# Optimization experiments

Measured on AMD Instinct MI355X. Metric: run time of the kernel, lower is better.

The kernel has to match this reference:

```python
import jax, jax.numpy as jnp
import numpy as np

L = 3          # encoder layers
H, D = 12, 64  # heads, head_dim
DM = H * D     # 768
DF = 3072
WH = WW = 14
S = WH * WW + 1            # 197 tokens incl. cls
ND = (2*WH-1)*(2*WW-1) + 3  # 732 rel-pos entries
EPS = 1e-12


def _make_rel_idx():
    coords = np.stack(np.meshgrid(np.arange(WH), np.arange(WW), indexing='ij'))
    coords = coords.reshape(2, -1)                      # [2, 196]
    rel = (coords[:, :, None] - coords[:, None, :]).transpose(1, 2, 0)  # [196,196,2]
    rel[:, :, 0] += WH - 1
    rel[:, :, 1] += WW - 1
    rel[:, :, 0] *= 2 * WW - 1
    idx = np.zeros((S, S), dtype=np.int32)
    idx[1:, 1:] = rel.sum(-1)
    idx[0, :] = ND - 3
    idx[:, 0] = ND - 2
    idx[0, 0] = ND - 1
    return jnp.asarray(idx.flatten())

REL_IDX = _make_rel_idx()


def _ln(x, g, b):
    m = jnp.mean(x, -1, keepdims=True)
    v = jnp.mean(jnp.square(x - m), -1, keepdims=True)
    return (x - m) * jax.lax.rsqrt(v + EPS) * g + b


def setup_inputs() -> dict:
    key = jax.random.key(0)
    ks = iter(jax.random.split(key, 32))
    p = lambda *s: jax.random.normal(next(ks), s, jnp.float32) * 0.02
    inp = {
        'x': jax.random.normal(next(ks), (64, WH, WW, DM), jnp.float32),
        'cls': p(1, 1, DM),
        'g1': jnp.ones((L, DM)), 'b1': jnp.zeros((L, DM)),
        'Wq': p(L, DM, DM), 'bq': jnp.zeros((L, DM)),
        'Wk': p(L, DM, DM),
        'Wv': p(L, DM, DM), 'bv': jnp.zeros((L, DM)),
        'rel_tbl': p(L, ND, H),
        'Wo': p(L, DM, DM), 'bo': jnp.zeros((L, DM)),
        'lam1': jnp.full((L, DM), 0.1),
        'g2': jnp.ones((L, DM)), 'b2': jnp.zeros((L, DM)),
        'Wi': p(L, DM, DF), 'bi': jnp.zeros((L, DF)),
        'Wmo': p(L, DF, DM), 'bmo': jnp.zeros((L, DM)),
        'lam2': jnp.full((L, DM), 0.1),
    }
    return inp


def reference(x, cls, g1, b1, Wq, bq, Wk, Wv, bv, rel_tbl, Wo, bo, lam1,
              g2, b2, Wi, bi, Wmo, bmo, lam2):
    B = x.shape[0]
    # patchemb: NHWC -> NCHW -> [B, C, HW] -> [B, HW, C], prepend cls token
    t = jnp.transpose(x, (0, 3, 1, 2)).reshape(B, DM, WH * WW)
    t = jnp.transpose(t, (0, 2, 1))
    h = jnp.concatenate([jnp.broadcast_to(cls, (B, 1, DM)), t], axis=1)  # [B,S,DM]

    scale = 1.0 / np.sqrt(D)
    for i in range(L):
        r = h
        hn = _ln(h, g1[i], b1[i])
        q = (hn @ Wq[i] + bq[i]).reshape(B, S, H, D)
        k = (hn @ Wk[i]).reshape(B, S, H, D)
        v = (hn @ Wv[i] + bv[i]).reshape(B, S, H, D)
        scores = jnp.einsum('bqhd,bkhd->bhqk', q, k) * scale   # [B,H,S,S]
        rel = rel_tbl[i][REL_IDX].reshape(S, S, H)             # gather bias table
        scores = scores + jnp.transpose(rel, (2, 0, 1))[None]
        probs = jax.nn.softmax(scores, axis=-1)
        ctx = jnp.einsum('bhqk,bkhd->bqhd', probs, v).reshape(B, S, DM)
        h = r + (ctx @ Wo[i] + bo[i]) * lam1[i]
        r = h
        hn = _ln(h, g2[i], b2[i])
        ff = jax.nn.gelu(hn @ Wi[i] + bi[i], approximate=False) @ Wmo[i] + bmo[i]
        h = r + ff * lam2[i]
    return h  # final encoder output [B, S, DM]
```

## Files before the change

### kernel.cpp

```cpp
#include <hip/hip_runtime.h>

#define DMM 768
#define DFF 3072
#define NH  12
#define HD  64
#define SQ  197
#define BA  64
#define NDD 732
#define MROWS (BA*SQ)
#define MPAD  12672
#define PCOLS 224
#define KS2   72
#define VTS   232
#define QS    2304

typedef unsigned short u16;
typedef __bf16 bf16x8 __attribute__((ext_vector_type(8)));
typedef float  f32x4  __attribute__((ext_vector_type(4)));
typedef unsigned short us8 __attribute__((ext_vector_type(8)));

__device__ __forceinline__ float b2f(u16 u) {
    unsigned v = ((unsigned)u) << 16;
    float f; __builtin_memcpy(&f, &v, 4); return f;
}
__device__ __forceinline__ u16 f2b(float f) {
    unsigned v; __builtin_memcpy(&v, &f, 4);
    unsigned r = v + 0x7FFFu + ((v >> 16) & 1u);
    return (u16)(r >> 16);
}
__device__ __forceinline__ float gelu_exact(float x) {
    return 0.5f * x * (1.0f + erff(x * 0.70710678118654752f));
}
__device__ __forceinline__ void gload16(const u16* g, u16* l) {
    __builtin_amdgcn_global_load_lds(
        (const __attribute__((address_space(1))) unsigned int*)(g),
        (__attribute__((address_space(3))) unsigned int*)(l), 16, 0, 0);
}
__device__ __forceinline__ void hard_barrier() {
    asm volatile("s_waitcnt lgkmcnt(0)" ::: "memory");
    __builtin_amdgcn_s_barrier();
}

__global__ void patch_k(const float* __restrict__ x, const float* __restrict__ cls,
                        float* __restrict__ h) {
    long idx = (long)blockIdx.x * 256 + threadIdx.x;
    if (idx >= (long)MPAD * DMM) return;
    long r = idx / DMM; int c = (int)(idx % DMM);
    float v = 0.0f;
    if (r < MROWS) {
        int b = (int)(r / SQ), s = (int)(r % SQ);
        v = (s == 0) ? cls[c] : x[((long)b * 196 + (s - 1)) * DMM + c];
    }
    h[idx] = v;
}

__global__ void out_k(const float* __restrict__ h, float* __restrict__ out) {
    long idx = (long)blockIdx.x * 256 + threadIdx.x;
    if (idx < (long)MROWS * DMM) out[idx] = h[idx];
}

__global__ __launch_bounds__(256) void tcast_k(const float* __restrict__ in,
                                               u16* __restrict__ out,
                                               int Kd, int Nd) {
    __shared__ float t[32][33];
    int k0 = blockIdx.x * 32, n0 = blockIdx.y * 32;
    int tx = threadIdx.x & 31, ty = threadIdx.x >> 5;
    #pragma unroll
    for (int i = 0; i < 4; ++i)
        t[tx][ty + 8 * i] = in[(long)(k0 + ty + 8 * i) * Nd + n0 + tx];
    __syncthreads();
    #pragma unroll
    for (int i = 0; i < 4; ++i)
        out[(long)(n0 + ty + 8 * i) * Kd + k0 + tx] = f2b(t[ty + 8 * i][tx]);
}

__global__ __launch_bounds__(256) void ln_k(const float* __restrict__ h,
                                            const float* __restrict__ g,
                                            const float* __restrict__ b,
                                            u16* __restrict__ hn) {
    int row = blockIdx.x, tid = threadIdx.x;
    const float* hr = h + (long)row * DMM;
    float x0 = hr[tid], x1 = hr[tid + 256], x2 = hr[tid + 512];
    float s = x0 + x1 + x2, sq = x0 * x0 + x1 * x1 + x2 * x2;
    #pragma unroll
    for (int m = 32; m > 0; m >>= 1) {
        s  += __shfl_xor(s,  m, 64);
        sq += __shfl_xor(sq, m, 64);
    }
    __shared__ float ls[4], lq[4];
    int w = tid >> 6;
    if ((tid & 63) == 0) { ls[w] = s; lq[w] = sq; }
    __syncthreads();
    s  = ls[0] + ls[1] + ls[2] + ls[3];
    sq = lq[0] + lq[1] + lq[2] + lq[3];
    float mean = s * (1.0f / DMM);
    float var  = fmaxf(sq * (1.0f / DMM) - mean * mean, 0.0f);
    float rs = rsqrtf(var + 1e-12f);
    u16* hnr = hn + (long)row * DMM;
    hnr[tid]       = f2b((x0 - mean) * rs * g[tid]       + b[tid]);
    hnr[tid + 256] = f2b((x1 - mean) * rs * g[tid + 256] + b[tid + 256]);
    hnr[tid + 512] = f2b((x2 - mean) * rs * g[tid + 512] + b[tid + 512]);
}

__global__ void bqkv_k(const float* __restrict__ bq, const float* __restrict__ bv,
                       float* __restrict__ out) {
    int i = blockIdx.x * 256 + threadIdx.x;
    if (i >= QS) return;
    out[i] = (i < 768) ? bq[i] : ((i < 1536) ? 0.0f : bv[i - 1536]);
}

template <int EPI>
__global__ __launch_bounds__(256) void gemm_bt(
    const u16* __restrict__ A, const u16* __restrict__ BT,
    const float* __restrict__ bias, u16* __restrict__ outB,
    float* __restrict__ hio, const float* __restrict__ lam,
    int K, int N) {
    __shared__ __align__(16) u16 pool[3 * 8192];
    int tid = threadIdx.x;
    int w = tid >> 6, lane = tid & 63;
    int wr = w >> 1, wc = w & 1;
    int m16 = lane & 15;
    int kq  = (lane >> 4) * 8;
    int kq4 = (lane >> 4) * 4;

    int nwg = gridDim.x, bid = blockIdx.x;
    int qd = nwg >> 3, rm = nwg & 7;
    int xcd = bid & 7, seq = bid >> 3;
    int wg = (xcd < rm ? xcd * (qd + 1) : rm * (qd + 1) + (xcd - rm) * qd) + seq;
    int ntn = N >> 7;
    long m0 = (long)(wg / ntn) * 128;
    long n0 = (long)(wg % ntn) * 128;

    f32x4 acc[4][4] = {};

    int row_a = tid >> 2;
    int col_a = (tid & 3) * 8;
    const u16* gA0 = &A[(m0 + row_a) * (long)K + col_a];
    const u16* gA1 = &A[(m0 + 64 + row_a) * (long)K + col_a];
    const u16* gB0 = &BT[(n0 + row_a) * (long)K + col_a];
    const u16* gB1 = &BT[(n0 + 64 + row_a) * (long)K + col_a];
    int wo = w * 512;

    auto stage = [&](int k, u16* buf) {
        int k0 = k << 5;
        gload16(gA0 + k0, buf + wo);
        gload16(gA1 + k0, buf + 2048 + wo);
        gload16(gB0 + k0, buf + 4096 + wo);
        gload16(gB1 + k0, buf + 6144 + wo);
    };
    auto compute = [&](const u16* buf) {
        bf16x8 af[4], bf[4];
        #pragma unroll
        for (int i = 0; i < 4; ++i)
            af[i] = *(const bf16x8*)&buf[(wr * 64 + i * 16 + m16) * 32 + kq];
        #pragma unroll
        for (int j = 0; j < 4; ++j)
            bf[j] = *(const bf16x8*)&buf[4096 + (wc * 64 + j * 16 + m16) * 32 + kq];
        #pragma unroll
        for (int i = 0; i < 4; ++i)
            #pragma unroll
            for (int j = 0; j < 4; ++j)
                acc[i][j] = __builtin_amdgcn_mfma_f32_16x16x32_bf16(
                    af[i], bf[j], acc[i][j], 0, 0, 0);
    };

    const int nsteps = K >> 5;
    stage(0, pool);
    stage(1, pool + 8192);
    u16* sb = pool + 16384;
    u16* cb = pool;
    for (int ks = 0; ks < nsteps - 2; ++ks) {
        asm volatile("s_waitcnt vmcnt(4) lgkmcnt(0)" ::: "memory");
        __builtin_amdgcn_s_barrier();
        stage(ks + 2, sb);
        compute(cb);
        sb = cb;
        cb = (cb == pool + 16384) ? pool : cb + 8192;
    }
    asm volatile("s_waitcnt vmcnt(4) lgkmcnt(0)" ::: "memory");
    __builtin_amdgcn_s_barrier();
    compute(cb);
    cb = (cb == pool + 16384) ? pool : cb + 8192;
    asm volatile("s_waitcnt vmcnt(0) lgkmcnt(0)" ::: "memory");
    __builtin_amdgcn_s_barrier();
    compute(cb);

    hard_barrier();
    float* Cs = (float*)pool;
    float bcol[4];
    #pragma unroll
    for (int j = 0; j < 4; ++j)
        bcol[j] = bias ? bias[n0 + wc * 64 + j * 16 + m16] : 0.0f;
    int et4 = tid * 4;
    int colr = et4 & 127;
    f32x4 lam4 = {};
    if (EPI == 2) lam4 = *(const f32x4*)&lam[n0 + colr];

    #pragma unroll
    for (int p = 0; p < 2; ++p) {
        if (p) hard_barrier();
        if (wr == p) {
            #pragma unroll
            for (int i = 0; i < 4; ++i)
                #pragma unroll
                for (int j = 0; j < 4; ++j)
                    #pragma unroll
                    for (int r = 0; r < 4; ++r)
                        Cs[(i * 16 + kq4 + r) * 132 + wc * 64 + j * 16 + m16] =
                            acc[i][j][r] + bcol[j];
        }
        hard_barrier();
        #pragma unroll
        for (int k = 0; k < 8; ++k) {
            int e0 = k * 1024 + et4;
            int row = e0 >> 7;
            f32x4 v = *(const f32x4*)&Cs[row * 132 + colr];
            long gi = (m0 + p * 64 + row) * (long)N + n0 + colr;
            if (EPI == 0) {
                uint2 o;
                o.x = (unsigned)f2b(v[0]) | ((unsigned)f2b(v[1]) << 16);
                o.y = (unsigned)f2b(v[2]) | ((unsigned)f2b(v[3]) << 16);
                *(uint2*)&outB[gi] = o;
            } else if (EPI == 1) {
                uint2 o;
                o.x = (unsigned)f2b(gelu_exact(v[0])) | ((unsigned)f2b(gelu_exact(v[1])) << 16);
                o.y = (unsigned)f2b(gelu_exact(v[2])) | ((unsigned)f2b(gelu_exact(v[3])) << 16);
                *(uint2*)&outB[gi] = o;
            } else {
                f32x4 hv = *(f32x4*)&hio[gi];
                #pragma unroll
                for (int t = 0; t < 4; ++t) hv[t] += v[t] * lam4[t];
                *(f32x4*)&hio[gi] = hv;
            }
        }
    }
}

__device__ __forceinline__ int relidx(int q, int k) {
    if (q == 0 && k == 0) return NDD - 1;
    if (k == 0) return NDD - 2;
    if (q == 0) return NDD - 3;
    int a = q - 1, c = k - 1;
    int dh = a / 14 - c / 14 + 13;
    int dw = a % 14 - c % 14 + 13;
    return dh * 27 + dw;
}

__global__ void bias_k(const float* __restrict__ rel, float* __restrict__ bias) {
    int idx = blockIdx.x * 256 + threadIdx.x;
    if (idx >= NH * 208 * 208) return;
    int hh = idx / (208 * 208);
    int r = (idx / 208) % 208, c = idx % 208;
    float v = 0.0f;
    if (r < SQ && c < SQ) v = rel[relidx(r, c) * NH + hh];
    bias[idx] = v;
}

__global__ __launch_bounds__(256) void attn_qk(
    const u16* __restrict__ QKV, const float* __restrict__ bias,
    u16* __restrict__ P) {
    int bh = blockIdx.x;
    int b = bh / NH, hh = bh % NH;
    __shared__ u16 Ks[208 * KS2];
    int tid = threadIdx.x, w = tid >> 6, lane = tid & 63;
    long base = ((long)b * SQ) * QS + hh * HD;
    const u16* Qp = QKV;
    const u16* Kp = QKV + 768;
    u16* Pb = P + (long)bh * 208 * PCOLS;
    for (int idx = tid; idx < 208 * 16; idx += 256)
        Pb[(idx >> 4) * PCOLS + 208 + (idx & 15)] = 0;
    for (int idx = tid; idx < 208 * 8; idx += 256) {
        int row = idx >> 3, dg = (idx & 7) * 8;
        us8 kv = {};
        if (row < SQ) kv = *(const us8*)&Kp[base + (long)row * QS + dg];
        *(us8*)&Ks[row * KS2 + dg] = kv;
    }
    __syncthreads();
    int m16 = lane & 15, quad = lane >> 4;
    int kq8 = quad * 8, q4 = quad * 4;
    const float* bh_bias = bias + (long)hh * 208 * 208;
    for (int t = w; t < 13; t += 4) {
        int m0 = t * 16;
        int qrow = m0 + m16; if (qrow > SQ - 1) qrow = SQ - 1;
        bf16x8 a0 = *(const bf16x8*)&Qp[base + (long)qrow * QS + kq8];
        bf16x8 a1 = *(const bf16x8*)&Qp[base + (long)qrow * QS + 32 + kq8];
        f32x4 sc[13];
        #pragma unroll
        for (int n = 0; n < 13; ++n) {
            bf16x8 b0 = *(const bf16x8*)&Ks[(n * 16 + m16) * KS2 + kq8];
            bf16x8 b1 = *(const bf16x8*)&Ks[(n * 16 + m16) * KS2 + 32 + kq8];
            f32x4 z = {};
            z = __builtin_amdgcn_mfma_f32_16x16x32_bf16(a0, b0, z, 0, 0, 0);
            z = __builtin_amdgcn_mfma_f32_16x16x32_bf16(a1, b1, z, 0, 0, 0);
            sc[n] = z;
        }
        float mx[4] = {-3e38f, -3e38f, -3e38f, -3e38f};
        #pragma unroll
        for (int n = 0; n < 13; ++n) {
            int col = n * 16 + m16;
            bool valid = col < SQ;
            #pragma unroll
            for (int r = 0; r < 4; ++r) {
                float v = sc[n][r] * 0.125f + bh_bias[(m0 + q4 + r) * 208 + col];
                v = valid ? v : -3e38f;
                sc[n][r] = v;
                mx[r] = fmaxf(mx[r], v);
            }
        }
        #pragma unroll
        for (int r = 0; r < 4; ++r)
            #pragma unroll
            for (int msk = 1; msk < 16; msk <<= 1)
                mx[r] = fmaxf(mx[r], __shfl_xor(mx[r], msk, 64));
        float sum[4] = {0, 0, 0, 0};
        #pragma unroll
        for (int n = 0; n < 13; ++n)
            #pragma unroll
            for (int r = 0; r < 4; ++r) {
                float e = __expf(sc[n][r] - mx[r]);
                sc[n][r] = e;
                sum[r] += e;
            }
        #pragma unroll
        for (int r = 0; r < 4; ++r)
            #pragma unroll
            for (int msk = 1; msk < 16; msk <<= 1)
                sum[r] += __shfl_xor(sum[r], msk, 64);
        float inv[4];
        #pragma unroll
        for (int r = 0; r < 4; ++r) inv[r] = 1.0f / sum[r];
        #pragma unroll
        for (int n = 0; n < 13; ++n) {
            int col = n * 16 + m16;
            #pragma unroll
            for (int r = 0; r < 4; ++r)
                Pb[(m0 + q4 + r) * PCOLS + col] = f2b(sc[n][r] * inv[r]);
        }
    }
}

__global__ __launch_bounds__(256) void attn_pv(
    const u16* __restrict__ P, const u16* __restrict__ QKV,
    u16* __restrict__ ctx) {
    int bh = blockIdx.x;
    int b = bh / NH, hh = bh % NH;
    __shared__ u16 Vt[64 * VTS];
    int tid = threadIdx.x, w = tid >> 6, lane = tid & 63;
    long base  = ((long)b * SQ) * QS + 1536 + hh * HD;
    long basec = ((long)b * SQ) * DMM + hh * HD;
    const u16* Vp = QKV;
    for (int idx = tid; idx < 224 * 8; idx += 256) {
        int row = idx >> 3, dg = (idx & 7) * 8;
        us8 vv = {};
        if (row < SQ) vv = *(const us8*)&Vp[base + (long)row * QS + dg];
        #pragma unroll
        for (int j = 0; j < 8; ++j) Vt[(dg + j) * VTS + row] = vv[j];
    }
    __syncthreads();
    const u16* Pb = P + (long)bh * 208 * PCOLS;
    int m16 = lane & 15, quad = lane >> 4;
    int kq8 = quad * 8, q4 = quad * 4;
    for (int t = w; t < 13; t += 4) {
        int m0 = t * 16;
        f32x4 co[4] = {};
        #pragma unroll
        for (int ks = 0; ks < 7; ++ks) {
            bf16x8 ap = *(const bf16x8*)&Pb[(m0 + m16) * PCOLS + ks * 32 + kq8];
            #pragma unroll
            for (int n = 0; n < 4; ++n) {
                bf16x8 bv = *(const bf16x8*)&Vt[(n * 16 + m16) * VTS + ks * 32 + kq8];
                co[n] = __builtin_amdgcn_mfma_f32_16x16x32_bf16(ap, bv, co[n], 0, 0, 0);
            }
        }
        #pragma unroll
        for (int n = 0; n < 4; ++n) {
            int col = n * 16 + m16;
            #pragma unroll
            for (int r = 0; r < 4; ++r) {
                int qr = m0 + q4 + r;
                if (qr < SQ) ctx[basec + (long)qr * DMM + col] = f2b(co[n][r]);
            }
        }
    }
}

extern "C" void kernel_launch(void* const* d_in, const int* in_sizes, int n_in,
                              void* d_out, int out_size, void* d_ws, size_t ws_size,
                              hipStream_t stream) {
    const float* x    = (const float*)d_in[0];
    const float* cls  = (const float*)d_in[1];
    const float* g1   = (const float*)d_in[2];
    const float* b1   = (const float*)d_in[3];
    const float* Wq   = (const float*)d_in[4];
    const float* bq   = (const float*)d_in[5];
    const float* Wk   = (const float*)d_in[6];
    const float* Wv   = (const float*)d_in[7];
    const float* bv   = (const float*)d_in[8];
    const float* rel  = (const float*)d_in[9];
    const float* Wo   = (const float*)d_in[10];
    const float* bo   = (const float*)d_in[11];
    const float* lam1 = (const float*)d_in[12];
    const float* g2   = (const float*)d_in[13];
    const float* b2   = (const float*)d_in[14];
    const float* Wi   = (const float*)d_in[15];
    const float* bi   = (const float*)d_in[16];
    const float* Wmo  = (const float*)d_in[17];
    const float* bmo  = (const float*)d_in[18];
    const float* lam2 = (const float*)d_in[19];

    char* p = (char*)d_ws;
    auto alloc = [&](size_t bytes) -> void* {
        void* r = (void*)p;
        p += (bytes + 255) & ~(size_t)255;
        return r;
    };
    float* h     = (float*)alloc((size_t)MPAD * DMM * 4);
    u16*   hn    = (u16*)alloc((size_t)MPAD * DMM * 2);
    u16*   qkvb  = (u16*)alloc((size_t)MPAD * QS * 2);
    u16*   ffh   = (u16*)alloc((size_t)MPAD * DFF * 2);
    u16*   WqkvT = (u16*)alloc((size_t)QS * DMM * 2);
    u16*   WoT   = (u16*)alloc((size_t)DMM * DMM * 2);
    u16*   WiT   = (u16*)alloc((size_t)DMM * DFF * 2);
    u16*   WmoT  = (u16*)alloc((size_t)DFF * DMM * 2);
    float* biasb = (float*)alloc((size_t)NH * 208 * 208 * 4);
    float* bqkv  = (float*)alloc((size_t)QS * 4);
    u16*   ctxb  = hn;
    u16*   Pbuf  = ffh;

    patch_k<<<((long)MPAD * DMM + 255) / 256, 256, 0, stream>>>(x, cls, h);

    dim3 tg1(DMM / 32, DMM / 32);
    dim3 tg2(DMM / 32, DFF / 32);
    dim3 tg3(DFF / 32, DMM / 32);
    int gqkv = (MPAD / 128) * (QS / 128);
    int g6   = (MPAD / 128) * (DMM / 128);
    int g24  = (MPAD / 128) * (DFF / 128);

    for (int i = 0; i < 3; ++i) {
        size_t wofs  = (size_t)i * DMM * DMM;
        size_t wofs2 = (size_t)i * DMM * DFF;
        tcast_k<<<tg1, 256, 0, stream>>>(Wq + wofs, WqkvT,                 DMM, DMM);
        tcast_k<<<tg1, 256, 0, stream>>>(Wk + wofs, WqkvT + 768 * DMM,     DMM, DMM);
        tcast_k<<<tg1, 256, 0, stream>>>(Wv + wofs, WqkvT + 2 * 768 * DMM, DMM, DMM);
        tcast_k<<<tg1, 256, 0, stream>>>(Wo + wofs, WoT, DMM, DMM);
        tcast_k<<<tg2, 256, 0, stream>>>(Wi + wofs2, WiT, DMM, DFF);
        tcast_k<<<tg3, 256, 0, stream>>>(Wmo + wofs2, WmoT, DFF, DMM);
        bias_k<<<(NH * 208 * 208 + 255) / 256, 256, 0, stream>>>(rel + (size_t)i * NDD * NH, biasb);
        bqkv_k<<<(QS + 255) / 256, 256, 0, stream>>>(bq + i * DMM, bv + i * DMM, bqkv);

        ln_k<<<MPAD, 256, 0, stream>>>(h, g1 + i * DMM, b1 + i * DMM, hn);
        gemm_bt<0><<<gqkv, 256, 0, stream>>>(hn, WqkvT, bqkv, qkvb, nullptr, nullptr, DMM, QS);
        attn_qk<<<BA * NH, 256, 0, stream>>>(qkvb, biasb, Pbuf);
        attn_pv<<<BA * NH, 256, 0, stream>>>(Pbuf, qkvb, ctxb);
        gemm_bt<2><<<g6, 256, 0, stream>>>(ctxb, WoT, bo + i * DMM, nullptr, h, lam1 + i * DMM, DMM, DMM);
        ln_k<<<MPAD, 256, 0, stream>>>(h, g2 + i * DMM, b2 + i * DMM, hn);
        gemm_bt<1><<<g24, 256, 0, stream>>>(hn, WiT, bi + i * DFF, ffh, nullptr, nullptr, DMM, DFF);
        gemm_bt<2><<<g6, 256, 0, stream>>>(ffh, WmoT, bmo + i * DMM, nullptr, h, lam2 + i * DMM, DFF, DMM);
    }

    out_k<<<((long)MROWS * DMM + 255) / 256, 256, 0, stream>>>(h, (float*)d_out);
}
```

Measured before the change: 1.471 ms.

## Switch GEMM from triple-buffered to double-buffered LDS pipeline

Replaces the three-slot rotating LDS buffer in the bf16 GEMM with two fixed buffers and an unrolled-by-two main loop. Each compute is now followed by a full barrier before its buffer is refilled. This shrinks the LDS footprint to about 33 KB, which may let more workgroups share a CU. The cost is a shallower prefetch (one tile ahead instead of two) and extra barriers per K step, so global load latency is less hidden.

Result: faster. 1.383 ms (-6.0%).

```diff
diff --git a/kernel.cpp b/kernel.cpp
--- a/kernel.cpp
+++ b/kernel.cpp
@@ -115,7 +115,7 @@
     const float* __restrict__ bias, u16* __restrict__ outB,
     float* __restrict__ hio, const float* __restrict__ lam,
     int K, int N) {
-    __shared__ __align__(16) u16 pool[3 * 8192];
+    __shared__ __align__(16) u16 pool[16896];
     int tid = threadIdx.x;
     int w = tid >> 6, lane = tid & 63;
     int wr = w >> 1, wc = w & 1;
@@ -140,6 +140,9 @@
     const u16* gB0 = &BT[(n0 + row_a) * (long)K + col_a];
     const u16* gB1 = &BT[(n0 + 64 + row_a) * (long)K + col_a];
     int wo = w * 512;
+
+    u16* const b0 = pool;
+    u16* const b1 = pool + 8192;
 
     auto stage = [&](int k, u16* buf) {
         int k0 = k << 5;
@@ -165,25 +168,27 @@
     };
 
     const int nsteps = K >> 5;
-    stage(0, pool);
-    stage(1, pool + 8192);
-    u16* sb = pool + 16384;
-    u16* cb = pool;
-    for (int ks = 0; ks < nsteps - 2; ++ks) {
-        asm volatile("s_waitcnt vmcnt(4) lgkmcnt(0)" ::: "memory");
+    stage(0, b0);
+    for (int ks = 0; ks < nsteps - 2; ks += 2) {
+        stage(ks + 1, b1);
+        asm volatile("s_waitcnt vmcnt(4)" ::: "memory");
         __builtin_amdgcn_s_barrier();
-        stage(ks + 2, sb);
-        compute(cb);
-        sb = cb;
-        cb = (cb == pool + 16384) ? pool : cb + 8192;
-    }
-    asm volatile("s_waitcnt vmcnt(4) lgkmcnt(0)" ::: "memory");
+        compute(b0);
+        hard_barrier();
+        stage(ks + 2, b0);
+        asm volatile("s_waitcnt vmcnt(4)" ::: "memory");
+        __builtin_amdgcn_s_barrier();
+        compute(b1);
+        hard_barrier();
+    }
+    stage(nsteps - 1, b1);
+    asm volatile("s_waitcnt vmcnt(4)" ::: "memory");
     __builtin_amdgcn_s_barrier();
-    compute(cb);
-    cb = (cb == pool + 16384) ? pool : cb + 8192;
-    asm volatile("s_waitcnt vmcnt(0) lgkmcnt(0)" ::: "memory");
+    compute(b0);
+    hard_barrier();
+    asm volatile("s_waitcnt vmcnt(0)" ::: "memory");
     __builtin_amdgcn_s_barrier();
-    compute(cb);
+    compute(b1);
 
     hard_barrier();
     float* Cs = (float*)pool;
```
